# Performance work log

Measured on AMD Instinct MI355X. Metric: run time of the kernel, lower is better.

The kernel has to match this reference:

```python
import jax, jax.numpy as jnp
import numpy as np

NUM_HEADS = 16
EMBED_DIM = 128
SEQ_LEN = 1024
BATCH = 4


def setup_inputs() -> dict:
    key = jax.random.key(0)
    ks = jax.random.split(key, 5)
    x = jax.random.normal(ks[0], (BATCH, SEQ_LEN, EMBED_DIM), dtype=jnp.float32)
    scale = 0.02
    w_q = jax.random.normal(ks[1], (NUM_HEADS * EMBED_DIM, EMBED_DIM), dtype=jnp.float32) * scale
    w_k = jax.random.normal(ks[2], (NUM_HEADS * EMBED_DIM, EMBED_DIM), dtype=jnp.float32) * scale
    w_v = jax.random.normal(ks[3], (NUM_HEADS * EMBED_DIM, EMBED_DIM), dtype=jnp.float32) * scale
    w_o = jax.random.normal(ks[4], (EMBED_DIM, NUM_HEADS * EMBED_DIM), dtype=jnp.float32) * scale
    return {"x": x, "w_q": w_q, "w_k": w_k, "w_v": w_v, "w_o": w_o}


def _rope_tables(seq_len, embed_dim, dtype):
    half = embed_dim // 2
    # faithful to source: angles = 10000 ** (2*i / embed_dim)  (positive exponent)
    angles = jnp.power(jnp.asarray(10000.0, dtype), 2.0 * jnp.arange(half, dtype=dtype) / embed_dim)
    theta = jnp.arange(seq_len, dtype=dtype)[:, None] * angles[None, :]  # [S, half]
    return jnp.cos(theta), jnp.sin(theta)


def _apply_rope(t, cos, sin):
    # t: [B, S, H, E] viewed as complex pairs on last dim
    B, S, H, E = t.shape
    tr = t.reshape(B, S, H, E // 2, 2)
    a, b = tr[..., 0], tr[..., 1]
    c = cos[None, :, None, :]
    s = sin[None, :, None, :]
    out = jnp.stack([a * c - b * s, a * s + b * c], axis=-1)
    return out.reshape(B, S, H, E)


def reference(x, w_q, w_k, w_v, w_o):
    B, S, E = x.shape
    H = NUM_HEADS
    q = jnp.einsum('bse,fe->bsf', x, w_q).reshape(B, S, H, E)
    k = jnp.einsum('bse,fe->bsf', x, w_k).reshape(B, S, H, E)
    v = jnp.einsum('bse,fe->bsf', x, w_v).reshape(B, S, H, E)
    cos, sin = _rope_tables(S, E, x.dtype)
    q = _apply_rope(q, cos, sin)
    k = _apply_rope(k, cos, sin)
    att = jnp.einsum('bqhd,bkhd->bhqk', q, k) / jnp.sqrt(jnp.asarray(E, x.dtype))
    causal = jnp.tril(jnp.ones((S, S), dtype=bool))[None, None]
    att = jnp.where(causal, att, jnp.asarray(-jnp.inf, x.dtype))
    att = jax.nn.softmax(att, axis=-1)
    y = jnp.einsum('bhqk,bkhd->bqhd', att, v).reshape(B, S, H * E)
    return jnp.einsum('bsf,ef->bse', y, w_o)
```

## Files before the change

### kernel.cpp

```cpp
#include <hip/hip_runtime.h>

typedef unsigned short u16;
typedef unsigned int   u32;
typedef __attribute__((ext_vector_type(8))) short bf8_t;
typedef __attribute__((ext_vector_type(4))) float f4_t;

#define SEQ   1024
#define NH    16
#define DH    128
#define BATCH 4
#define MROWS 4096
#define FDIM  2048

__device__ __forceinline__ u16 f2bf(float f) {
  union { float f; u32 u; } v; v.f = f;
  u32 u = v.u;
  u += 0x7fffu + ((u >> 16) & 1u);
  return (u16)(u >> 16);
}

__global__ __launch_bounds__(256) void prep(
    const float* __restrict__ x,  const float* __restrict__ wq,
    const float* __restrict__ wk, const float* __restrict__ wv,
    const float* __restrict__ wo,
    u16* __restrict__ xb, u16* __restrict__ wqb, u16* __restrict__ wkb,
    u16* __restrict__ wvb, u16* __restrict__ wob,
    float* __restrict__ cosT, float* __restrict__ sinT) {
  const int gb = blockIdx.x;
  if (gb < 768) {
    int i = gb * 256 + threadIdx.x;
    const float* s; u16* d; int o;
    if      (i <  65536) { s = x;  d = xb;  o = i; }
    else if (i <  98304) { s = wq; d = wqb; o = i - 65536; }
    else if (i < 131072) { s = wk; d = wkb; o = i - 98304; }
    else if (i < 163840) { s = wv; d = wvb; o = i - 131072; }
    else                 { s = wo; d = wob; o = i - 163840; }
    const f4_t* sp = reinterpret_cast<const f4_t*>(s + (size_t)o * 8);
    f4_t a = sp[0], b = sp[1];
    bf8_t pk;
#pragma unroll
    for (int j = 0; j < 4; ++j) { pk[j] = (short)f2bf(a[j]); pk[4 + j] = (short)f2bf(b[j]); }
    *reinterpret_cast<bf8_t*>(d + (size_t)o * 8) = pk;
  } else {
    int i = (gb - 768) * 256 + threadIdx.x;
    int p = i >> 10, s = i & 1023;
    float ef = (float)(2 * p) / 128.0f;
    float angf = (float)pow(10000.0, (double)ef);
    float thf  = (float)s * angf;
    cosT[i] = cosf(thf);
    sinT[i] = sinf(thf);
  }
}

__global__ __launch_bounds__(256) void qkv_rope(
    const u16* __restrict__ xb,
    const u16* __restrict__ wqb, const u16* __restrict__ wkb,
    const u16* __restrict__ wvb,
    const float* __restrict__ cosT, const float* __restrict__ sinT,
    u16* __restrict__ qo, u16* __restrict__ ko, u16* __restrict__ vo) {
  __shared__ __align__(16) u16 a_lds[64 * 128];
  __shared__ __align__(16) u16 b_lds[64 * 128];
  const int tid = threadIdx.x;
  const int mt = blockIdx.x;
  const int by = blockIdx.y;
  const int mat = by >> 5;
  const int nt  = by & 31;
  const u16* w = (mat == 0) ? wqb : ((mat == 1) ? wkb : wvb);
  const int m0 = mt * 64, n0 = nt * 64;

#pragma unroll
  for (int i = 0; i < 4; ++i) {
    int idx = tid + i * 256;
    int row = idx >> 4, e0 = (idx & 15) * 8;
    int hw = ((row << 7) | e0) ^ ((row & 7) << 3);
    bf8_t xa = *reinterpret_cast<const bf8_t*>(xb + (size_t)(m0 + row) * 128 + e0);
    *reinterpret_cast<bf8_t*>(&a_lds[hw]) = xa;
    bf8_t wa = *reinterpret_cast<const bf8_t*>(w + (size_t)(n0 + row) * 128 + e0);
    *reinterpret_cast<bf8_t*>(&b_lds[hw]) = wa;
  }
  __syncthreads();

  const int lane = tid & 63, wid = tid >> 6;
  const int wr = wid >> 1, wc = wid & 1;
  const int g = lane >> 4, c16 = lane & 15;
  f4_t acc[2][2];
#pragma unroll
  for (int a = 0; a < 2; ++a)
#pragma unroll
    for (int b = 0; b < 2; ++b) acc[a][b] = (f4_t)0.0f;

#pragma unroll
  for (int kc = 0; kc < 4; ++kc) {
    bf8_t af[2], bf_[2];
#pragma unroll
    for (int fr = 0; fr < 2; ++fr) {
      int row = wr * 32 + fr * 16 + c16;
      int hw = ((row << 7) | (kc * 32 + g * 8)) ^ ((row & 7) << 3);
      af[fr] = *reinterpret_cast<const bf8_t*>(&a_lds[hw]);
    }
#pragma unroll
    for (int fc = 0; fc < 2; ++fc) {
      int row = wc * 32 + fc * 16 + c16;
      int hw = ((row << 7) | (kc * 32 + g * 8)) ^ ((row & 7) << 3);
      bf_[fc] = *reinterpret_cast<const bf8_t*>(&b_lds[hw]);
    }
#pragma unroll
    for (int fr = 0; fr < 2; ++fr)
#pragma unroll
      for (int fc = 0; fc < 2; ++fc)
        acc[fr][fc] = __builtin_amdgcn_mfma_f32_16x16x32_bf16(af[fr], bf_[fc], acc[fr][fc], 0, 0, 0);
  }

  if (mat == 2) {
    __syncthreads();
#pragma unroll
    for (int fr = 0; fr < 2; ++fr)
#pragma unroll
      for (int fc = 0; fc < 2; ++fc)
#pragma unroll
        for (int j = 0; j < 4; ++j) {
          int fcol = wc * 32 + fc * 16 + c16;
          int m = wr * 32 + fr * 16 + g * 4 + j;
          a_lds[fcol * 72 + m] = f2bf(acc[fr][fc][j]);
        }
    __syncthreads();
    const int b = mt >> 4, sl0 = m0 & 1023;
    const int hq = nt >> 1, dvb = (nt & 1) * 64;
#pragma unroll
    for (int i = 0; i < 2; ++i) {
      int r = tid >> 2, c0 = ((tid & 3) * 2 + i) * 8;
      bf8_t v = *reinterpret_cast<const bf8_t*>(&a_lds[r * 72 + c0]);
      size_t adr = ((size_t)((b * 16 + hq) * 128 + dvb + r)) * 1024 + sl0 + c0;
      *reinterpret_cast<bf8_t*>(vo + adr) = v;
    }
    return;
  }

  u16* outp = (mat == 0) ? qo : ko;
#pragma unroll
  for (int fr = 0; fr < 2; ++fr) {
#pragma unroll
    for (int fc = 0; fc < 2; ++fc) {
      int fcol = n0 + wc * 32 + fc * 16 + c16;
      int h = fcol >> 7, d = fcol & 127, p = d >> 1;
      int m_base = m0 + wr * 32 + fr * 16 + g * 4;
      int b = m_base >> 10, sl_base = m_base & 1023;
      f4_t cv4 = *reinterpret_cast<const f4_t*>(&cosT[p * 1024 + sl_base]);
      f4_t sv4 = *reinterpret_cast<const f4_t*>(&sinT[p * 1024 + sl_base]);
#pragma unroll
      for (int j = 0; j < 4; ++j) {
        float v = acc[fr][fc][j];
        float vx = __shfl_xor(v, 1);
        float cv = cv4[j], sv = sv4[j];
        if (!(lane & 1)) {
          float e_out = v * cv - vx * sv;
          float o_out = v * sv + vx * cv;
          u32 u = (u32)f2bf(e_out) | ((u32)f2bf(o_out) << 16);
          u32 elem = ((u32)((b * 16 + h) * 1024 + (sl_base + j))) * 128 + (u32)d;
          reinterpret_cast<u32*>(outp)[elem >> 1] = u;
        }
      }
    }
  }
}

__device__ __forceinline__ void stage_load(const u16* __restrict__ Kp,
                                           const u16* __restrict__ Vt, int t,
                                           int tid, bf8_t kreg[4], bf8_t vreg[4]) {
#pragma unroll
  for (int i = 0; i < 4; ++i) {
    int n = tid >> 2, c0 = ((tid & 3) * 4 + i) * 8;
    kreg[i] = *reinterpret_cast<const bf8_t*>(Kp + (size_t)(t * 64 + n) * 128 + c0);
    int dv = tid >> 1, c1 = ((tid & 1) * 4 + i) * 8;
    vreg[i] = *reinterpret_cast<const bf8_t*>(Vt + (size_t)dv * 1024 + t * 64 + c1);
  }
}
__device__ __forceinline__ void stage_write(int tid, const bf8_t kreg[4],
                                            const bf8_t vreg[4],
                                            u16* k_lds, u16* vT) {
#pragma unroll
  for (int i = 0; i < 4; ++i) {
    int n = tid >> 2, c0 = ((tid & 3) * 4 + i) * 8;
    *reinterpret_cast<bf8_t*>(&k_lds[n * 128 + (c0 ^ ((n & 7) << 3))]) = kreg[i];
    int dv = tid >> 1, c1 = ((tid & 1) * 4 + i) * 8;
    *reinterpret_cast<bf8_t*>(&vT[dv * 72 + c1]) = vreg[i];
  }
}

__global__ __launch_bounds__(256, 3) void attn(
    const u16* __restrict__ qw, const u16* __restrict__ kw,
    const u16* __restrict__ vtg, u16* __restrict__ yw) {
  __shared__ __align__(16) u16 k_lds[64 * 128];
  __shared__ __align__(16) u16 vT[144 * 72];
  __shared__ __align__(16) u16 p_lds[4][16 * 64];
  const int tid = threadIdx.x, lane = tid & 63, wid = tid >> 6;
  const int g = lane >> 4, c16 = lane & 15;
  const int bid = blockIdx.x;
  const int pp = 15 - (bid >> 6);
  const int bh = bid & 63;
  const int b = bh >> 4, h = bh & 15;
  const int qt = 2 * pp + (wid >> 1);
  const int T = pp + 1;
  const u16* Qp = qw + (size_t)bh * SEQ * DH;
  const u16* Kp = kw + (size_t)bh * SEQ * DH;
  const u16* Vt = vtg + (size_t)bh * DH * SEQ;
  const float kscale = 0.08838834764831845f * 1.4426950408889634f;
  const int qrow0 = qt * 32 + (wid & 1) * 16;
  const int moff = (wid >> 1) * 32 + (wid & 1) * 16;

  {
    int r = 128 + (tid >> 4), c0 = (tid & 15) * 4;
    u16 v = (r == 128) ? (u16)0x3F80 : (u16)0;
#pragma unroll
    for (int e = 0; e < 4; ++e) vT[r * 72 + c0 + e] = v;
  }

  bf8_t qf[4];
#pragma unroll
  for (int c = 0; c < 4; ++c)
    qf[c] = *reinterpret_cast<const bf8_t*>(Qp + (size_t)(qrow0 + c16) * 128 + c * 32 + g * 8);

  f4_t yacc[9];
#pragma unroll
  for (int f = 0; f < 9; ++f) yacc[f] = (f4_t)0.0f;
  float m_run[4];
#pragma unroll
  for (int j = 0; j < 4; ++j) m_run[j] = -3e38f;

  {
    bf8_t k0[4], v0[4];
    stage_load(Kp, Vt, 0, tid, k0, v0);
    stage_write(tid, k0, v0, k_lds, vT);
  }
  __syncthreads();

  for (int t = 0; t < T; ++t) {
    const bool pf = (t + 1 < T);
    bf8_t kreg[4], vreg[4];
    if (pf) stage_load(Kp, Vt, t + 1, tid, kreg, vreg);

    f4_t sf[4];
#pragma unroll
    for (int nf = 0; nf < 4; ++nf) sf[nf] = (f4_t)0.0f;
    __builtin_amdgcn_s_setprio(1);
#pragma unroll
    for (int nf = 0; nf < 4; ++nf) {
      int row = nf * 16 + c16;
#pragma unroll
      for (int kc = 0; kc < 4; ++kc) {
        int hw = ((row << 7) | (kc * 32 + g * 8)) ^ ((row & 7) << 3);
        bf8_t kf = *reinterpret_cast<const bf8_t*>(&k_lds[hw]);
        sf[nf] = __builtin_amdgcn_mfma_f32_16x16x32_bf16(qf[kc], kf, sf[nf], 0, 0, 0);
      }
    }
    __builtin_amdgcn_s_setprio(0);

    if (t == T - 1) {
#pragma unroll
      for (int nf = 0; nf < 4; ++nf) {
        int keyc = nf * 16 + c16;
#pragma unroll
        for (int j = 0; j < 4; ++j)
          if (keyc > moff + g * 4 + j) sf[nf][j] = -3e38f;
      }
    }

    int chk = 0;
#pragma unroll
    for (int j = 0; j < 4; ++j) {
      float lmx = fmaxf(fmaxf(sf[0][j], sf[1][j]), fmaxf(sf[2][j], sf[3][j]));
      chk |= (lmx > m_run[j] + 32.0f) ? 1 : 0;
    }
    if (__any(chk)) {
      float lm[4];
#pragma unroll
      for (int j = 0; j < 4; ++j) {
        lm[j] = fmaxf(fmaxf(sf[0][j], sf[1][j]), fmaxf(sf[2][j], sf[3][j]));
        lm[j] = fmaxf(lm[j], __shfl_xor(lm[j], 1));
        lm[j] = fmaxf(lm[j], __shfl_xor(lm[j], 2));
        lm[j] = fmaxf(lm[j], __shfl_xor(lm[j], 4));
        lm[j] = fmaxf(lm[j], __shfl_xor(lm[j], 8));
      }
#pragma unroll
      for (int j = 0; j < 4; ++j) {
        float mn = fmaxf(m_run[j], lm[j]);
        float alpha = exp2f((m_run[j] - mn) * kscale);
        m_run[j] = mn;
#pragma unroll
        for (int f = 0; f < 9; ++f) yacc[f][j] *= alpha;
      }
    }

#pragma unroll
    for (int nf = 0; nf < 4; ++nf) {
#pragma unroll
      for (int j = 0; j < 4; ++j) {
        float pv = exp2f((sf[nf][j] - m_run[j]) * kscale);
        int q = g * 4 + j, n = nf * 16 + c16;
        int hw = ((q << 6) | n) ^ ((q & 7) << 3);
        p_lds[wid][hw] = f2bf(pv);
      }
    }
    bf8_t pa[2];
#pragma unroll
    for (int cc = 0; cc < 2; ++cc) {
      int hw = ((c16 << 6) | (cc * 32 + g * 8)) ^ ((c16 & 7) << 3);
      pa[cc] = *reinterpret_cast<const bf8_t*>(&p_lds[wid][hw]);
    }

    __builtin_amdgcn_s_setprio(1);
#pragma unroll
    for (int f = 0; f < 9; ++f) {
#pragma unroll
      for (int cc = 0; cc < 2; ++cc) {
        bf8_t vf = *reinterpret_cast<const bf8_t*>(&vT[(f * 16 + c16) * 72 + cc * 32 + g * 8]);
        yacc[f] = __builtin_amdgcn_mfma_f32_16x16x32_bf16(pa[cc], vf, yacc[f], 0, 0, 0);
      }
    }
    __builtin_amdgcn_s_setprio(0);

    __syncthreads();
    if (pf) {
      stage_write(tid, kreg, vreg, k_lds, vT);
      __syncthreads();
    }
  }

  float rl[4];
#pragma unroll
  for (int j = 0; j < 4; ++j) {
    float lv = __shfl(yacc[8][j], lane & 48);
    rl[j] = 1.0f / lv;
  }
#pragma unroll
  for (int f = 0; f < 8; ++f) {
#pragma unroll
    for (int j = 0; j < 4; ++j) {
      float yv = yacc[f][j] * rl[j];
      float yn = __shfl_xor(yv, 1);
      if (!(lane & 1)) {
        int s_ = qrow0 + g * 4 + j;
        int dv = f * 16 + c16;
        u32 u = (u32)f2bf(yv) | ((u32)f2bf(yn) << 16);
        u32 elem = ((u32)(b * 1024 + s_)) * 2048 + (u32)(h * 128 + dv);
        reinterpret_cast<u32*>(yw)[elem >> 1] = u;
      }
    }
  }
}

__global__ __launch_bounds__(256) void oproj(
    const u16* __restrict__ yw, const u16* __restrict__ wob,
    float* __restrict__ out) {
  __shared__ __align__(16) u16 a_lds[64 * 64];
  __shared__ __align__(16) u16 b_lds[64 * 64];
  const int tid = threadIdx.x, lane = tid & 63, wid = tid >> 6;
  const int g = lane >> 4, c16 = lane & 15;
  const int wr = wid >> 1, wc = wid & 1;
  const int m0 = blockIdx.x * 64, n0 = blockIdx.y * 64;
  const int z = blockIdx.z;
  const int kt0 = z * 16;
  f4_t acc[2][2];
#pragma unroll
  for (int a = 0; a < 2; ++a)
#pragma unroll
    for (int b = 0; b < 2; ++b) acc[a][b] = (f4_t)0.0f;

  const int srow = tid >> 3, sk0 = (tid & 7) * 8;

  bf8_t areg[2], breg[2];
#pragma unroll
  for (int i = 0; i < 2; ++i) {
    int row = srow + i * 32;
    areg[i] = *reinterpret_cast<const bf8_t*>(yw + (size_t)(m0 + row) * 2048 + kt0 * 64 + sk0);
    breg[i] = *reinterpret_cast<const bf8_t*>(wob + (size_t)(n0 + row) * 2048 + kt0 * 64 + sk0);
  }
#pragma unroll
  for (int i = 0; i < 2; ++i) {
    int row = srow + i * 32;
    int hw = ((row << 6) | sk0) ^ ((row & 7) << 3);
    *reinterpret_cast<bf8_t*>(&a_lds[hw]) = areg[i];
    *reinterpret_cast<bf8_t*>(&b_lds[hw]) = breg[i];
  }
  __syncthreads();

  for (int kt = kt0; kt < kt0 + 16; ++kt) {
    const bool pf = (kt + 1 < kt0 + 16);
    if (pf) {
      int kb = (kt + 1) * 64;
#pragma unroll
      for (int i = 0; i < 2; ++i) {
        int row = srow + i * 32;
        areg[i] = *reinterpret_cast<const bf8_t*>(yw + (size_t)(m0 + row) * 2048 + kb + sk0);
        breg[i] = *reinterpret_cast<const bf8_t*>(wob + (size_t)(n0 + row) * 2048 + kb + sk0);
      }
    }
#pragma unroll
    for (int c = 0; c < 2; ++c) {
      bf8_t af[2], bf_[2];
#pragma unroll
      for (int fr = 0; fr < 2; ++fr) {
        int row = wr * 32 + fr * 16 + c16;
        int hw = ((row << 6) | (c * 32 + g * 8)) ^ ((row & 7) << 3);
        af[fr] = *reinterpret_cast<const bf8_t*>(&a_lds[hw]);
      }
#pragma unroll
      for (int fc = 0; fc < 2; ++fc) {
        int row = wc * 32 + fc * 16 + c16;
        int hw = ((row << 6) | (c * 32 + g * 8)) ^ ((row & 7) << 3);
        bf_[fc] = *reinterpret_cast<const bf8_t*>(&b_lds[hw]);
      }
#pragma unroll
      for (int fr = 0; fr < 2; ++fr)
#pragma unroll
        for (int fc = 0; fc < 2; ++fc)
          acc[fr][fc] = __builtin_amdgcn_mfma_f32_16x16x32_bf16(af[fr], bf_[fc], acc[fr][fc], 0, 0, 0);
    }
    __syncthreads();
    if (pf) {
#pragma unroll
      for (int i = 0; i < 2; ++i) {
        int row = srow + i * 32;
        int hw = ((row << 6) | sk0) ^ ((row & 7) << 3);
        *reinterpret_cast<bf8_t*>(&a_lds[hw]) = areg[i];
        *reinterpret_cast<bf8_t*>(&b_lds[hw]) = breg[i];
      }
      __syncthreads();
    }
  }
#pragma unroll
  for (int fr = 0; fr < 2; ++fr)
#pragma unroll
    for (int fc = 0; fc < 2; ++fc)
#pragma unroll
      for (int j = 0; j < 4; ++j) {
        int m = m0 + wr * 32 + fr * 16 + g * 4 + j;
        int e = n0 + wc * 32 + fc * 16 + c16;
        atomicAdd(&out[(size_t)m * 128 + e], acc[fr][fc][j]);
      }
}

extern "C" void kernel_launch(void* const* d_in, const int* in_sizes, int n_in,
                              void* d_out, int out_size, void* d_ws, size_t ws_size,
                              hipStream_t stream) {
  const float* x  = (const float*)d_in[0];
  const float* wq = (const float*)d_in[1];
  const float* wk = (const float*)d_in[2];
  const float* wv = (const float*)d_in[3];
  const float* wo = (const float*)d_in[4];
  float* out = (float*)d_out;

  char* ws = (char*)d_ws;
  const size_t NEED = (512ull << 10) + 4ull * (16ull << 20) + (3ull << 20);
  if (ws_size < NEED) return;
  float* cosT = (float*)ws;
  float* sinT = cosT + 64 * 1024;
  u16* qws = (u16*)(ws + (512 << 10));
  u16* kws = qws + (8u << 20);
  u16* vws = kws + (8u << 20);
  u16* yws = vws + (8u << 20);
  u16* xb  = yws + (8u << 20);
  u16* wqb = xb  + (1u << 19);
  u16* wkb = wqb + (1u << 18);
  u16* wvb = wkb + (1u << 18);
  u16* wob = wvb + (1u << 18);

  hipMemsetAsync(d_out, 0, (size_t)out_size * sizeof(float), stream);
  prep<<<1024, 256, 0, stream>>>(x, wq, wk, wv, wo, xb, wqb, wkb, wvb, wob, cosT, sinT);
  qkv_rope<<<dim3(64, 96), 256, 0, stream>>>(xb, wqb, wkb, wvb, cosT, sinT, qws, kws, vws);
  attn<<<1024, 256, 0, stream>>>(qws, kws, vws, yws);
  oproj<<<dim3(64, 2, 2), 256, 0, stream>>>(yws, wob, out);
}
```

Before: 100.6 us.

## Reuse x tile across Q/K/V in one block; drop attention K/V register prefetch

The QKV projection kernel now has each block load the x tile once and loop over the three weight matrices. This cuts the grid from 96 to 32 column tiles and removes repeated x loads. Separately, the attention kernel no longer prefetches the next K/V tile into registers during compute. It now loads and writes K/V to LDS after the barrier, which lowers register pressure but exposes the global-load latency on every iteration. The projection kernel also gets fewer blocks, and so less parallelism.

After: 91.79 us, median of 2. 1.1x faster.

```diff
diff --git a/kernel.cpp b/kernel.cpp
--- a/kernel.cpp
+++ b/kernel.cpp
@@ -52,6 +52,18 @@
   }
 }
 
+__device__ __forceinline__ void stage_tile(const u16* __restrict__ src,
+                                           u16* __restrict__ dst, int tid) {
+#pragma unroll
+  for (int i = 0; i < 4; ++i) {
+    int idx = tid + i * 256;
+    int row = idx >> 4, e0 = (idx & 15) * 8;
+    int hw = ((row << 7) | e0) ^ ((row & 7) << 3);
+    *reinterpret_cast<bf8_t*>(&dst[hw]) =
+        *reinterpret_cast<const bf8_t*>(src + (size_t)row * 128 + e0);
+  }
+}
+
 __global__ __launch_bounds__(256) void qkv_rope(
     const u16* __restrict__ xb,
     const u16* __restrict__ wqb, const u16* __restrict__ wkb,
@@ -62,128 +74,114 @@
   __shared__ __align__(16) u16 b_lds[64 * 128];
   const int tid = threadIdx.x;
   const int mt = blockIdx.x;
-  const int by = blockIdx.y;
-  const int mat = by >> 5;
-  const int nt  = by & 31;
-  const u16* w = (mat == 0) ? wqb : ((mat == 1) ? wkb : wvb);
+  const int nt = blockIdx.y;
   const int m0 = mt * 64, n0 = nt * 64;
 
-#pragma unroll
-  for (int i = 0; i < 4; ++i) {
-    int idx = tid + i * 256;
-    int row = idx >> 4, e0 = (idx & 15) * 8;
-    int hw = ((row << 7) | e0) ^ ((row & 7) << 3);
-    bf8_t xa = *reinterpret_cast<const bf8_t*>(xb + (size_t)(m0 + row) * 128 + e0);
-    *reinterpret_cast<bf8_t*>(&a_lds[hw]) = xa;
-    bf8_t wa = *reinterpret_cast<const bf8_t*>(w + (size_t)(n0 + row) * 128 + e0);
-    *reinterpret_cast<bf8_t*>(&b_lds[hw]) = wa;
-  }
-  __syncthreads();
+  stage_tile(xb + (size_t)m0 * 128, a_lds, tid);
 
   const int lane = tid & 63, wid = tid >> 6;
   const int wr = wid >> 1, wc = wid & 1;
   const int g = lane >> 4, c16 = lane & 15;
-  f4_t acc[2][2];
-#pragma unroll
-  for (int a = 0; a < 2; ++a)
-#pragma unroll
-    for (int b = 0; b < 2; ++b) acc[a][b] = (f4_t)0.0f;
-
-#pragma unroll
-  for (int kc = 0; kc < 4; ++kc) {
-    bf8_t af[2], bf_[2];
-#pragma unroll
-    for (int fr = 0; fr < 2; ++fr) {
-      int row = wr * 32 + fr * 16 + c16;
-      int hw = ((row << 7) | (kc * 32 + g * 8)) ^ ((row & 7) << 3);
-      af[fr] = *reinterpret_cast<const bf8_t*>(&a_lds[hw]);
-    }
-#pragma unroll
-    for (int fc = 0; fc < 2; ++fc) {
-      int row = wc * 32 + fc * 16 + c16;
-      int hw = ((row << 7) | (kc * 32 + g * 8)) ^ ((row & 7) << 3);
-      bf_[fc] = *reinterpret_cast<const bf8_t*>(&b_lds[hw]);
-    }
-#pragma unroll
-    for (int fr = 0; fr < 2; ++fr)
-#pragma unroll
-      for (int fc = 0; fc < 2; ++fc)
-        acc[fr][fc] = __builtin_amdgcn_mfma_f32_16x16x32_bf16(af[fr], bf_[fc], acc[fr][fc], 0, 0, 0);
-  }
-
-  if (mat == 2) {
+
+#pragma unroll
+  for (int mat = 0; mat < 3; ++mat) {
+    if (mat) __syncthreads();
+    const u16* w = (mat == 0) ? wqb : ((mat == 1) ? wkb : wvb);
+    stage_tile(w + (size_t)n0 * 128, b_lds, tid);
     __syncthreads();
-#pragma unroll
-    for (int fr = 0; fr < 2; ++fr)
-#pragma unroll
-      for (int fc = 0; fc < 2; ++fc)
-#pragma unroll
-        for (int j = 0; j < 4; ++j) {
-          int fcol = wc * 32 + fc * 16 + c16;
-          int m = wr * 32 + fr * 16 + g * 4 + j;
-          a_lds[fcol * 72 + m] = f2bf(acc[fr][fc][j]);
+
+    f4_t acc[2][2];
+#pragma unroll
+    for (int a = 0; a < 2; ++a)
+#pragma unroll
+      for (int b = 0; b < 2; ++b) acc[a][b] = (f4_t)0.0f;
+
+#pragma unroll
+    for (int kc = 0; kc < 4; ++kc) {
+      bf8_t af[2], bf_[2];
+#pragma unroll
+      for (int fr = 0; fr < 2; ++fr) {
+        int row = wr * 32 + fr * 16 + c16;
+        int hw = ((row << 7) | (kc * 32 + g * 8)) ^ ((row & 7) << 3);
+        af[fr] = *reinterpret_cast<const bf8_t*>(&a_lds[hw]);
+      }
+#pragma unroll
+      for (int fc = 0; fc < 2; ++fc) {
+        int row = wc * 32 + fc * 16 + c16;
+        int hw = ((row << 7) | (kc * 32 + g * 8)) ^ ((row & 7) << 3);
+        bf_[fc] = *reinterpret_cast<const bf8_t*>(&b_lds[hw]);
+      }
+#pragma unroll
+      for (int fr = 0; fr < 2; ++fr)
+#pragma unroll
+        for (int fc = 0; fc < 2; ++fc)
+          acc[fr][fc] = __builtin_amdgcn_mfma_f32_16x16x32_bf16(af[fr], bf_[fc], acc[fr][fc], 0, 0, 0);
+    }
+
+    if (mat == 2) {
+      __syncthreads();
+#pragma unroll
+      for (int fr = 0; fr < 2; ++fr)
+#pragma unroll
+        for (int fc = 0; fc < 2; ++fc)
+#pragma unroll
+          for (int j = 0; j < 4; ++j) {
+            int fcol = wc * 32 + fc * 16 + c16;
+            int m = wr * 32 + fr * 16 + g * 4 + j;
+            a_lds[fcol * 72 + m] = f2bf(acc[fr][fc][j]);
+          }
+      __syncthreads();
+      const int b = mt >> 4, sl0 = m0 & 1023;
+      const int hq = nt >> 1, dvb = (nt & 1) * 64;
+#pragma unroll
+      for (int i = 0; i < 2; ++i) {
+        int r = tid >> 2, c0 = ((tid & 3) * 2 + i) * 8;
+        bf8_t v = *reinterpret_cast<const bf8_t*>(&a_lds[r * 72 + c0]);
+        size_t adr = ((size_t)((b * 16 + hq) * 128 + dvb + r)) * 1024 + sl0 + c0;
+        *reinterpret_cast<bf8_t*>(vo + adr) = v;
+      }
+    } else {
+      u16* outp = (mat == 0) ? qo : ko;
+#pragma unroll
+      for (int fr = 0; fr < 2; ++fr) {
+#pragma unroll
+        for (int fc = 0; fc < 2; ++fc) {
+          int fcol = n0 + wc * 32 + fc * 16 + c16;
+          int h = fcol >> 7, d = fcol & 127, p = d >> 1;
+          int m_base = m0 + wr * 32 + fr * 16 + g * 4;
+          int b = m_base >> 10, sl_base = m_base & 1023;
+          f4_t cv4 = *reinterpret_cast<const f4_t*>(&cosT[p * 1024 + sl_base]);
+          f4_t sv4 = *reinterpret_cast<const f4_t*>(&sinT[p * 1024 + sl_base]);
+#pragma unroll
+          for (int j = 0; j < 4; ++j) {
+            float v = acc[fr][fc][j];
+            float vx = __shfl_xor(v, 1);
+            float cv = cv4[j], sv = sv4[j];
+            if (!(lane & 1)) {
+              float e_out = v * cv - vx * sv;
+              float o_out = v * sv + vx * cv;
+              u32 u = (u32)f2bf(e_out) | ((u32)f2bf(o_out) << 16);
+              u32 elem = ((u32)((b * 16 + h) * 1024 + (sl_base + j))) * 128 + (u32)d;
+              reinterpret_cast<u32*>(outp)[elem >> 1] = u;
+            }
+          }
         }
-    __syncthreads();
-    const int b = mt >> 4, sl0 = m0 & 1023;
-    const int hq = nt >> 1, dvb = (nt & 1) * 64;
-#pragma unroll
-    for (int i = 0; i < 2; ++i) {
-      int r = tid >> 2, c0 = ((tid & 3) * 2 + i) * 8;
-      bf8_t v = *reinterpret_cast<const bf8_t*>(&a_lds[r * 72 + c0]);
-      size_t adr = ((size_t)((b * 16 + hq) * 128 + dvb + r)) * 1024 + sl0 + c0;
-      *reinterpret_cast<bf8_t*>(vo + adr) = v;
-    }
-    return;
-  }
-
-  u16* outp = (mat == 0) ? qo : ko;
-#pragma unroll
-  for (int fr = 0; fr < 2; ++fr) {
-#pragma unroll
-    for (int fc = 0; fc < 2; ++fc) {
-      int fcol = n0 + wc * 32 + fc * 16 + c16;
-      int h = fcol >> 7, d = fcol & 127, p = d >> 1;
-      int m_base = m0 + wr * 32 + fr * 16 + g * 4;
-      int b = m_base >> 10, sl_base = m_base & 1023;
-      f4_t cv4 = *reinterpret_cast<const f4_t*>(&cosT[p * 1024 + sl_base]);
-      f4_t sv4 = *reinterpret_cast<const f4_t*>(&sinT[p * 1024 + sl_base]);
-#pragma unroll
-      for (int j = 0; j < 4; ++j) {
-        float v = acc[fr][fc][j];
-        float vx = __shfl_xor(v, 1);
-        float cv = cv4[j], sv = sv4[j];
-        if (!(lane & 1)) {
-          float e_out = v * cv - vx * sv;
-          float o_out = v * sv + vx * cv;
-          u32 u = (u32)f2bf(e_out) | ((u32)f2bf(o_out) << 16);
-          u32 elem = ((u32)((b * 16 + h) * 1024 + (sl_base + j))) * 128 + (u32)d;
-          reinterpret_cast<u32*>(outp)[elem >> 1] = u;
-        }
-      }
-    }
-  }
-}
-
-__device__ __forceinline__ void stage_load(const u16* __restrict__ Kp,
-                                           const u16* __restrict__ Vt, int t,
-                                           int tid, bf8_t kreg[4], bf8_t vreg[4]) {
+      }
+    }
+  }
+}
+
+__device__ __forceinline__ void stage_kv(const u16* __restrict__ Kp,
+                                         const u16* __restrict__ Vt, int t,
+                                         int tid, u16* k_lds, u16* vT) {
 #pragma unroll
   for (int i = 0; i < 4; ++i) {
     int n = tid >> 2, c0 = ((tid & 3) * 4 + i) * 8;
-    kreg[i] = *reinterpret_cast<const bf8_t*>(Kp + (size_t)(t * 64 + n) * 128 + c0);
+    bf8_t kv = *reinterpret_cast<const bf8_t*>(Kp + (size_t)(t * 64 + n) * 128 + c0);
+    *reinterpret_cast<bf8_t*>(&k_lds[n * 128 + (c0 ^ ((n & 7) << 3))]) = kv;
     int dv = tid >> 1, c1 = ((tid & 1) * 4 + i) * 8;
-    vreg[i] = *reinterpret_cast<const bf8_t*>(Vt + (size_t)dv * 1024 + t * 64 + c1);
-  }
-}
-__device__ __forceinline__ void stage_write(int tid, const bf8_t kreg[4],
-                                            const bf8_t vreg[4],
-                                            u16* k_lds, u16* vT) {
-#pragma unroll
-  for (int i = 0; i < 4; ++i) {
-    int n = tid >> 2, c0 = ((tid & 3) * 4 + i) * 8;
-    *reinterpret_cast<bf8_t*>(&k_lds[n * 128 + (c0 ^ ((n & 7) << 3))]) = kreg[i];
-    int dv = tid >> 1, c1 = ((tid & 1) * 4 + i) * 8;
-    *reinterpret_cast<bf8_t*>(&vT[dv * 72 + c1]) = vreg[i];
+    bf8_t vv = *reinterpret_cast<const bf8_t*>(Vt + (size_t)dv * 1024 + t * 64 + c1);
+    *reinterpret_cast<bf8_t*>(&vT[dv * 72 + c1]) = vv;
   }
 }
 
@@ -227,18 +225,10 @@
 #pragma unroll
   for (int j = 0; j < 4; ++j) m_run[j] = -3e38f;
 
-  {
-    bf8_t k0[4], v0[4];
-    stage_load(Kp, Vt, 0, tid, k0, v0);
-    stage_write(tid, k0, v0, k_lds, vT);
-  }
+  stage_kv(Kp, Vt, 0, tid, k_lds, vT);
   __syncthreads();
 
   for (int t = 0; t < T; ++t) {
-    const bool pf = (t + 1 < T);
-    bf8_t kreg[4], vreg[4];
-    if (pf) stage_load(Kp, Vt, t + 1, tid, kreg, vreg);
-
     f4_t sf[4];
 #pragma unroll
     for (int nf = 0; nf < 4; ++nf) sf[nf] = (f4_t)0.0f;
@@ -320,8 +310,8 @@
     __builtin_amdgcn_s_setprio(0);
 
     __syncthreads();
-    if (pf) {
-      stage_write(tid, kreg, vreg, k_lds, vT);
+    if (t + 1 < T) {
+      stage_kv(Kp, Vt, t + 1, tid, k_lds, vT);
       __syncthreads();
     }
   }
@@ -467,7 +457,7 @@
 
   hipMemsetAsync(d_out, 0, (size_t)out_size * sizeof(float), stream);
   prep<<<1024, 256, 0, stream>>>(x, wq, wk, wv, wo, xb, wqb, wkb, wvb, wob, cosT, sinT);
-  qkv_rope<<<dim3(64, 96), 256, 0, stream>>>(xb, wqb, wkb, wvb, cosT, sinT, qws, kws, vws);
+  qkv_rope<<<dim3(64, 32), 256, 0, stream>>>(xb, wqb, wkb, wvb, cosT, sinT, qws, kws, vws);
   attn<<<1024, 256, 0, stream>>>(qws, kws, vws, yws);
   oproj<<<dim3(64, 2, 2), 256, 0, stream>>>(yws, wob, out);
 }
```
